# Optimization experiments

Measured on AMD Instinct MI355X. Metric: run time of the kernel, lower is better.

## Reference

```python
import jax, jax.numpy as jnp
import numpy as np

NUM_CLASSES = 19
EPS = 1e-8  # torch cosine_similarity eps


def setup_inputs() -> dict:
    key = jax.random.key(0)
    k1, k2 = jax.random.split(key)
    inputs = jax.random.normal(k1, (8, 64, 512, 512), dtype=jnp.float32)
    targets = jax.random.randint(k2, (8, 512, 512), 0, NUM_CLASSES, dtype=jnp.int64)
    return {"inputs": inputs, "targets": targets}


def reference(inputs, targets):
    K = NUM_CLASSES
    B, C, H, W = inputs.shape
    # Flatten pixels: [N, C] features, [N] labels
    x = inputs.transpose(0, 2, 3, 1).reshape(-1, C)
    t = targets.reshape(-1)
    # Per-class centroids via one scatter-sum (replaces the per-class mask loop)
    sums = jax.ops.segment_sum(x, t, num_segments=K)  # [K, C]
    counts = jax.ops.segment_sum(jnp.ones_like(t, dtype=x.dtype), t, num_segments=K)  # [K]
    centers = sums / jnp.maximum(counts, 1.0)[:, None]  # [K, C]
    # Pairwise cosine similarity (torch clamps each norm by eps)
    norms = jnp.maximum(jnp.sqrt(jnp.sum(centers * centers, axis=1)), EPS)
    cn = centers / norms[:, None]
    S = cn @ cn.T  # [K, K] cosine sim matrix
    # CosineEmbeddingLoss: y=+1 (diag) -> 1 - cos; y=-1 -> max(0, cos).
    # Original: sum_i mean_j loss_ij, then / K^2  ==  sum_ij loss_ij / K^3
    eye = jnp.eye(K, dtype=bool)
    per_pair = jnp.where(eye, 1.0 - S, jnp.maximum(S, 0.0))
    return jnp.sum(per_pair) / (K * K * K)
```

## Files before the change

### kernel.cpp

```cpp
#include <hip/hip_runtime.h>

#define NK 19
#define NC 64
#define HW (512*512)
#define NB 8
#define BLOCK 256
#define PIX_PER_BLOCK 1024
#define NBLOCKS ((NB*HW)/PIX_PER_BLOCK)
#define NCOPIES 16
#define SUMS (NK*NC)
#define COPY_STRIDE 1280

__global__ __launch_bounds__(BLOCK) void accum_kernel(
    const float* __restrict__ x, const int* __restrict__ t,
    float* __restrict__ ws) {
  __shared__ float acc[4][SUMS];
  __shared__ float cnt[4][32];

  const int tid = threadIdx.x;
  const int wv  = tid >> 6;

  for (int i = tid; i < 4 * SUMS; i += BLOCK) ((float*)acc)[i] = 0.0f;
  if (tid < 128) ((float*)cnt)[tid] = 0.0f;
  __syncthreads();

  const int bid   = blockIdx.x;
  const int batch = bid >> 8;
  const int hw    = ((bid & 255) << 10) + (tid << 2);

  const int4 lbl = *reinterpret_cast<const int4*>(t + (bid << 10) + (tid << 2));
  const int t0 = lbl.x, t1 = lbl.y, t2 = lbl.z, t3 = lbl.w;

  float* cw = cnt[wv];
  atomicAdd(cw + t0, 1.0f);
  atomicAdd(cw + t1, 1.0f);
  atomicAdd(cw + t2, 1.0f);
  atomicAdd(cw + t3, 1.0f);

  const float4* p0 =
      reinterpret_cast<const float4*>(x + (size_t)batch * (NC * HW) + hw);
  float* aw = acc[wv];

#pragma unroll 2
  for (int c = 0; c < NC; c += 4) {
    float4 v0 = p0[(size_t)(c + 0) * (HW / 4)];
    float4 v1 = p0[(size_t)(c + 1) * (HW / 4)];
    float4 v2 = p0[(size_t)(c + 2) * (HW / 4)];
    float4 v3 = p0[(size_t)(c + 3) * (HW / 4)];
    float* A;
    A = aw + (c + 0) * NK;
    atomicAdd(A + t0, v0.x); atomicAdd(A + t1, v0.y);
    atomicAdd(A + t2, v0.z); atomicAdd(A + t3, v0.w);
    A = aw + (c + 1) * NK;
    atomicAdd(A + t0, v1.x); atomicAdd(A + t1, v1.y);
    atomicAdd(A + t2, v1.z); atomicAdd(A + t3, v1.w);
    A = aw + (c + 2) * NK;
    atomicAdd(A + t0, v2.x); atomicAdd(A + t1, v2.y);
    atomicAdd(A + t2, v2.z); atomicAdd(A + t3, v2.w);
    A = aw + (c + 3) * NK;
    atomicAdd(A + t0, v3.x); atomicAdd(A + t1, v3.y);
    atomicAdd(A + t2, v3.z); atomicAdd(A + t3, v3.w);
  }

  __syncthreads();

  float* base = ws + (size_t)(bid & (NCOPIES - 1)) * COPY_STRIDE;
  for (int i = tid; i < SUMS; i += BLOCK) {
    float s = acc[0][i] + acc[1][i] + acc[2][i] + acc[3][i];
    atomicAdd(base + i, s);
  }
  if (tid < NK) {
    float s = cnt[0][tid] + cnt[1][tid] + cnt[2][tid] + cnt[3][tid];
    atomicAdd(base + SUMS + tid, s);
  }
}

__global__ __launch_bounds__(512) void finalize_kernel(
    const float* __restrict__ ws, float* __restrict__ out) {
  __shared__ float cen[NC * 20];
  __shared__ float invn[NK];
  __shared__ float cc[NK];
  __shared__ float red[8];

  const int tid = threadIdx.x;

  if (tid < NK) {
    float s = 0.0f;
    for (int r = 0; r < NCOPIES; ++r) s += ws[r * COPY_STRIDE + SUMS + tid];
    cc[tid] = fmaxf(s, 1.0f);
  }
  __syncthreads();

  for (int i = tid; i < SUMS; i += 512) {
    int c = i / NK, k = i - c * NK;
    float s = 0.0f;
    for (int r = 0; r < NCOPIES; ++r) s += ws[r * COPY_STRIDE + i];
    cen[c * 20 + k] = s / cc[k];
  }
  __syncthreads();

  if (tid < NK) {
    float sq = 0.0f;
    for (int c = 0; c < NC; ++c) {
      float v = cen[c * 20 + tid];
      sq += v * v;
    }
    invn[tid] = 1.0f / fmaxf(sqrtf(sq), 1e-8f);
  }
  __syncthreads();

  float contrib = 0.0f;
  if (tid < NK * NK) {
    int i = tid / NK, j = tid - (tid / NK) * NK;
    float dot = 0.0f;
    for (int c = 0; c < NC; ++c) dot += cen[c * 20 + i] * cen[c * 20 + j];
    float S = dot * invn[i] * invn[j];
    contrib = (i == j) ? (1.0f - S) : fmaxf(S, 0.0f);
  }

  for (int off = 32; off > 0; off >>= 1) contrib += __shfl_down(contrib, off, 64);
  if ((tid & 63) == 0) red[tid >> 6] = contrib;
  __syncthreads();
  if (tid == 0) {
    float s = 0.0f;
    for (int w = 0; w < 8; ++w) s += red[w];
    out[0] = s / 6859.0f;
  }
}

extern "C" void kernel_launch(void* const* d_in, const int* in_sizes, int n_in,
                              void* d_out, int out_size, void* d_ws, size_t ws_size,
                              hipStream_t stream) {
  const float* x = (const float*)d_in[0];
  const int*   t = (const int*)d_in[1];
  float* ws = (float*)d_ws;

  hipMemsetAsync(d_ws, 0, (size_t)NCOPIES * COPY_STRIDE * sizeof(float), stream);
  accum_kernel<<<NBLOCKS, BLOCK, 0, stream>>>(x, t, ws);
  finalize_kernel<<<1, 512, 0, stream>>>(ws, (float*)d_out);
}
```

Measured before the change: 1.223 ms.

## Stage channel tiles in shared memory to cut LDS atomic contention per channel

```diff
diff --git a/kernel.cpp b/kernel.cpp
--- a/kernel.cpp
+++ b/kernel.cpp
@@ -3,75 +3,89 @@
 #define NK 19
 #define NC 64
 #define HW (512*512)
-#define NB 8
 #define BLOCK 256
 #define PIX_PER_BLOCK 1024
-#define NBLOCKS ((NB*HW)/PIX_PER_BLOCK)
+#define NTILES 16
+#define NBLOCKS 2048
 #define NCOPIES 16
 #define SUMS (NK*NC)
 #define COPY_STRIDE 1280
+#define TROW 65
 
 __global__ __launch_bounds__(BLOCK) void accum_kernel(
     const float* __restrict__ x, const int* __restrict__ t,
     float* __restrict__ ws) {
-  __shared__ float acc[4][SUMS];
-  __shared__ float cnt[4][32];
+  __shared__ float tile[NC * TROW];
+  __shared__ float bins[SUMS];
+  __shared__ int   lbl[PIX_PER_BLOCK];
+  __shared__ float cnt[8][NK];
 
   const int tid = threadIdx.x;
-  const int wv  = tid >> 6;
+  const int bid = blockIdx.x;
+  const int batch   = bid >> 8;
+  const int pixbase = (bid & 255) << 10;
 
-  for (int i = tid; i < 4 * SUMS; i += BLOCK) ((float*)acc)[i] = 0.0f;
-  if (tid < 128) ((float*)cnt)[tid] = 0.0f;
+  for (int i = tid; i < SUMS; i += BLOCK) bins[i] = 0.0f;
+  if (tid < 8 * NK) ((float*)cnt)[tid] = 0.0f;
   __syncthreads();
 
-  const int bid   = blockIdx.x;
-  const int batch = bid >> 8;
-  const int hw    = ((bid & 255) << 10) + (tid << 2);
+  {
+    const int4 l4 = *reinterpret_cast<const int4*>(
+        t + (size_t)batch * HW + pixbase + tid * 4);
+    *reinterpret_cast<int4*>(&lbl[tid * 4]) = l4;
+    float* cr = cnt[tid & 7];
+    atomicAdd(cr + l4.x, 1.0f);
+    atomicAdd(cr + l4.y, 1.0f);
+    atomicAdd(cr + l4.z, 1.0f);
+    atomicAdd(cr + l4.w, 1.0f);
+  }
 
-  const int4 lbl = *reinterpret_cast<const int4*>(t + (bid << 10) + (tid << 2));
-  const int t0 = lbl.x, t1 = lbl.y, t2 = lbl.z, t3 = lbl.w;
+  const int r = tid >> 2;
+  const int s = tid & 3;
+  const float* xrow = x + (size_t)(batch * NC + r) * HW + pixbase;
+  float* tdst = &tile[r * TROW];
 
-  float* cw = cnt[wv];
-  atomicAdd(cw + t0, 1.0f);
-  atomicAdd(cw + t1, 1.0f);
-  atomicAdd(cw + t2, 1.0f);
-  atomicAdd(cw + t3, 1.0f);
+  const int wv = tid >> 6;
+  const int ln = tid & 63;
+  const int my_c = wv * 16 + (ln & 15);
+  const int pg = ln >> 4;
+  float* bc = &bins[my_c * NK];
 
-  const float4* p0 =
-      reinterpret_cast<const float4*>(x + (size_t)batch * (NC * HW) + hw);
-  float* aw = acc[wv];
+  for (int tl = 0; tl < NTILES; ++tl) {
+    const float* src = xrow + tl * 64 + s * 4;
+    const float4 v0 = *reinterpret_cast<const float4*>(src + 0);
+    const float4 v1 = *reinterpret_cast<const float4*>(src + 16);
+    const float4 v2 = *reinterpret_cast<const float4*>(src + 32);
+    const float4 v3 = *reinterpret_cast<const float4*>(src + 48);
+    __syncthreads();
+    float* dst = tdst + s * 4;
+    *reinterpret_cast<float4*>(dst + 0)  = v0;
+    *reinterpret_cast<float4*>(dst + 16) = v1;
+    *reinterpret_cast<float4*>(dst + 32) = v2;
+    *reinterpret_cast<float4*>(dst + 48) = v3;
+    __syncthreads();
 
-#pragma unroll 2
-  for (int c = 0; c < NC; c += 4) {
-    float4 v0 = p0[(size_t)(c + 0) * (HW / 4)];
-    float4 v1 = p0[(size_t)(c + 1) * (HW / 4)];
-    float4 v2 = p0[(size_t)(c + 2) * (HW / 4)];
-    float4 v3 = p0[(size_t)(c + 3) * (HW / 4)];
-    float* A;
-    A = aw + (c + 0) * NK;
-    atomicAdd(A + t0, v0.x); atomicAdd(A + t1, v0.y);
-    atomicAdd(A + t2, v0.z); atomicAdd(A + t3, v0.w);
-    A = aw + (c + 1) * NK;
-    atomicAdd(A + t0, v1.x); atomicAdd(A + t1, v1.y);
-    atomicAdd(A + t2, v1.z); atomicAdd(A + t3, v1.w);
-    A = aw + (c + 2) * NK;
-    atomicAdd(A + t0, v2.x); atomicAdd(A + t1, v2.y);
-    atomicAdd(A + t2, v2.z); atomicAdd(A + t3, v2.w);
-    A = aw + (c + 3) * NK;
-    atomicAdd(A + t0, v3.x); atomicAdd(A + t1, v3.y);
-    atomicAdd(A + t2, v3.z); atomicAdd(A + t3, v3.w);
+    const float* trow = &tile[my_c * TROW + pg * 16];
+    const int*   lrow = &lbl[tl * 64 + pg * 16];
+#pragma unroll
+    for (int j = 0; j < 4; ++j) {
+      const float4 xv = *reinterpret_cast<const float4*>(trow + j * 4);
+      const int4   t4 = *reinterpret_cast<const int4*>(lrow + j * 4);
+      atomicAdd(bc + t4.x, xv.x);
+      atomicAdd(bc + t4.y, xv.y);
+      atomicAdd(bc + t4.z, xv.z);
+      atomicAdd(bc + t4.w, xv.w);
+    }
   }
 
   __syncthreads();
 
   float* base = ws + (size_t)(bid & (NCOPIES - 1)) * COPY_STRIDE;
-  for (int i = tid; i < SUMS; i += BLOCK) {
-    float s = acc[0][i] + acc[1][i] + acc[2][i] + acc[3][i];
-    atomicAdd(base + i, s);
-  }
+  for (int i = tid; i < SUMS; i += BLOCK) atomicAdd(base + i, bins[i]);
   if (tid < NK) {
-    float s = cnt[0][tid] + cnt[1][tid] + cnt[2][tid] + cnt[3][tid];
-    atomicAdd(base + SUMS + tid, s);
+    float sc = 0.0f;
+    for (int rr = 0; rr < 8; ++rr) sc += cnt[rr][tid];
+    atomicAdd(base + SUMS + tid, sc);
   }
 }
 
```

Measured after the change: 1.318 ms. 1.08x slower.
